# Kernel optimization log

Measured on AMD Instinct MI355X. Metric: run time of the kernel, lower is better.

Reference implementation:

```python
import jax, jax.numpy as jnp
import numpy as np

HEADS = 8
D_MODEL = 512

def setup_inputs() -> dict:
    key = jax.random.key(0)
    ks = jax.random.split(key, 7)
    t, w, h, b = 8, 14, 14, 8
    seq = t * w * h + 1  # 1569, includes CLS token
    q = jax.random.normal(ks[0], (seq, b, D_MODEL), jnp.float32)
    k = jax.random.normal(ks[1], (seq, b, D_MODEL), jnp.float32)
    value = jax.random.normal(ks[2], (seq, b, D_MODEL), jnp.float32)
    in_proj_weight = jax.random.normal(ks[3], (3 * D_MODEL, D_MODEL), jnp.float32) * (D_MODEL ** -0.5)
    in_proj_bias = jax.random.normal(ks[4], (3 * D_MODEL,), jnp.float32) * 0.02
    out_w = jax.random.normal(ks[5], (D_MODEL, D_MODEL), jnp.float32) * (D_MODEL ** -0.5)
    out_b = jax.random.normal(ks[6], (D_MODEL,), jnp.float32) * 0.02
    return {"q": q, "k": k, "value": value,
            "in_proj_weight": in_proj_weight, "in_proj_bias": in_proj_bias,
            "out_w": out_w, "out_b": out_b, "t": t, "w": w, "h": h}

def _sdpa(q, k, v):
    # scaled dot-product attention over batched 3D tensors [B, L, dh]
    temp = q.shape[-1] ** 0.5
    scores = jnp.einsum('bqd,bkd->bqk', q, k) / temp
    a = jax.nn.softmax(scores, axis=-1)  # softmax over dim=2 == last dim
    return jnp.einsum('bqk,bkd->bqd', a, v), a

def reference(q, k, value, in_proj_weight, in_proj_bias, out_w, out_b, t, w, h):
    seq, b, c = q.shape
    H, dh, wh = HEADS, c // HEADS, w * h
    q_cls = q[:1]          # [1, b, c] passed through untouched
    x = q[1:]              # [t*wh, b, c]
    qkv = x @ in_proj_weight.T + in_proj_bias  # fused QKV proj
    qq, kk, vv = qkv[..., :c], qkv[..., c:2 * c], qkv[..., 2 * c:]
    to5 = lambda z: z.reshape(t, wh, b, H, dh)
    # spatial stage: batch = (H, b, t), attend over wh
    q_s = to5(qq).transpose(3, 2, 0, 1, 4).reshape(H * b * t, wh, dh)
    k_s = to5(kk).transpose(3, 2, 0, 1, 4).reshape(H * b * t, wh, dh)
    v_s = to5(vv).transpose(3, 2, 0, 1, 4).reshape(H * b * t, wh, dh)
    out_s, attn = _sdpa(q_s, k_s, v_s)
    # temporal stage: batch = (H, b, wh), attend over t; V comes from spatial output
    v_t = out_s.reshape(H, b, t, wh, dh).transpose(0, 1, 3, 2, 4).reshape(H * b * wh, t, dh)
    q_t = to5(qq).transpose(3, 2, 1, 0, 4).reshape(H * b * wh, t, dh)
    k_t = to5(kk).transpose(3, 2, 1, 0, 4).reshape(H * b * wh, t, dh)
    out_t, _ = _sdpa(q_t, k_t, v_t)
    # back to [t*wh, b, c]
    out = out_t.reshape(H, b, wh, t, dh).transpose(3, 2, 1, 0, 4).reshape(t * wh, b, c)
    out = out @ out_w.T + out_b
    return jnp.concatenate([q_cls, out], axis=0), attn
```

## Files before the change

kernel.cpp:

```cpp
#include <hip/hip_runtime.h>
#include <cstdint>
#include <cstddef>

typedef __bf16 bf16;
typedef __bf16 bf16x8 __attribute__((ext_vector_type(8)));
typedef __bf16 bf16x4 __attribute__((ext_vector_type(4)));
typedef float  f32x4  __attribute__((ext_vector_type(4)));

#define MFMA16(a, b, c) __builtin_amdgcn_mfma_f32_16x16x32_bf16(a, b, c, 0, 0, 0)

__device__ __forceinline__ void gl2lds16(const bf16* g, bf16* l) {
  __builtin_amdgcn_global_load_lds(
      (const __attribute__((address_space(1))) void*)g,
      (__attribute__((address_space(3))) void*)l, 16, 0, 0);
}

__device__ __forceinline__ void cvt4(const float* __restrict__ s, bf16* __restrict__ d) {
  f32x4 v = *(const f32x4*)s;
  bf16x4 o;
  o[0] = (bf16)v[0]; o[1] = (bf16)v[1]; o[2] = (bf16)v[2]; o[3] = (bf16)v[3];
  *(bf16x4*)d = o;
}

__global__ __launch_bounds__(256) void prep_kernel(
    const float* __restrict__ q, const float* __restrict__ win,
    const float* __restrict__ wout, float* __restrict__ out0,
    bf16* __restrict__ xb, bf16* __restrict__ wqb, bf16* __restrict__ wob) {
  long u = (long)blockIdx.x * 256 + threadIdx.x;
  const long NX4 = 1605632, NWQ4 = 196608, NWO4 = 65536, NQC4 = 1024;
  if (u < NX4) { cvt4(q + 4096 + u * 4, xb + u * 4); return; }
  u -= NX4;
  if (u < NWQ4) { cvt4(win + u * 4, wqb + u * 4); return; }
  u -= NWQ4;
  if (u < NWO4) { cvt4(wout + u * 4, wob + u * 4); return; }
  u -= NWO4;
  if (u < NQC4) { *(f32x4*)(out0 + u * 4) = *(const f32x4*)(q + u * 4); }
}

template <bool OUTF32>
__global__ __launch_bounds__(256) void gemm_bt(
    const bf16* __restrict__ A, const bf16* __restrict__ Bm,
    const float* __restrict__ bias, bf16* __restrict__ Qh,
    bf16* __restrict__ Kh, bf16* __restrict__ Vh,
    float* __restrict__ Cf, int N, int K, long coff) {
  __shared__ bf16 As[128 * 64];
  __shared__ bf16 Bs[128 * 64];
  const int tid = threadIdx.x;
  const int wid = tid >> 6, lane = tid & 63;
  const int lr = lane & 15, lg = lane >> 4;

  const int nwg = gridDim.x * gridDim.y;
  const int orig = blockIdx.y * gridDim.x + blockIdx.x;
  const int cpx = nwg >> 3;
  const int swz = (orig & 7) * cpx + (orig >> 3);
  const int m0 = (swz / gridDim.x) * 128;
  const int n0 = (swz % gridDim.x) * 128;

  const int wr = wid >> 1, wc = wid & 1;
  const int slot = lane & 7, r8 = lane >> 3;
  const int chunk = slot ^ r8;
  const int x7 = lr & 7;

  f32x4 acc[4][4] = {};

  for (int kt = 0; kt < K; kt += 64) {
    __syncthreads();
#pragma unroll
    for (int j = 0; j < 4; ++j) {
      int blk = wid * 4 + j;
      int row = blk * 8 + r8;
      gl2lds16(A + (size_t)(m0 + row) * K + kt + chunk * 8, As + blk * 512);
      gl2lds16(Bm + (size_t)(n0 + row) * K + kt + chunk * 8, Bs + blk * 512);
    }
    __syncthreads();

#pragma unroll
    for (int kk = 0; kk < 2; ++kk) {
      bf16x8 af[4], bfr[4];
#pragma unroll
      for (int m = 0; m < 4; ++m)
        af[m] = *(const bf16x8*)(As + (wr * 64 + m * 16 + lr) * 64 +
                                 (((kk * 4 + lg) ^ x7) * 8));
#pragma unroll
      for (int n = 0; n < 4; ++n)
        bfr[n] = *(const bf16x8*)(Bs + (wc * 64 + n * 16 + lr) * 64 +
                                  (((kk * 4 + lg) ^ x7) * 8));
#pragma unroll
      for (int m = 0; m < 4; ++m)
#pragma unroll
        for (int n = 0; n < 4; ++n)
          acc[m][n] = MFMA16(af[m], bfr[n], acc[m][n]);
    }
  }

  if (OUTF32) {
#pragma unroll
    for (int m = 0; m < 4; ++m) {
      int row = m0 + wr * 64 + m * 16 + lg * 4;
#pragma unroll
      for (int n = 0; n < 4; ++n) {
        int col = n0 + wc * 64 + n * 16 + lr;
        float bv = bias[col];
#pragma unroll
        for (int i = 0; i < 4; ++i)
          __builtin_nontemporal_store(
              acc[m][n][i] + bv, Cf + coff + (size_t)(row + i) * N + col);
      }
    }
  } else {
    int off[4][4];
#pragma unroll
    for (int m = 0; m < 4; ++m)
#pragma unroll
      for (int i = 0; i < 4; ++i) {
        int r = m0 + wr * 64 + m * 16 + lg * 4 + i;
        int ti2 = r / 1568, rem = r - ti2 * 1568;
        off[m][i] = (int)(((rem & 7) * 8 + ti2) * 12544 + (rem >> 3) * 64);
      }
#pragma unroll
    for (int n = 0; n < 4; ++n) {
      int col = n0 + wc * 64 + n * 16 + lr;
      float bv = bias[col];
      int sec = col >> 9, c = col & 511;
      int hh = c >> 6, dd = c & 63;
      bf16* base = (sec == 0 ? Qh : (sec == 1 ? Kh : Vh)) +
                   (size_t)hh * 802816 + dd;
#pragma unroll
      for (int m = 0; m < 4; ++m)
#pragma unroll
        for (int i = 0; i < 4; ++i)
          base[off[m][i]] = (bf16)(acc[m][n][i] + bv);
    }
  }
}

__global__ __launch_bounds__(1024) void spatial_attn(
    const bf16* __restrict__ Qh, const bf16* __restrict__ Kh,
    const bf16* __restrict__ Vh, float* __restrict__ attn_out,
    bf16* __restrict__ outs) {
  __shared__ bf16 Kl[224 * 64];
  __shared__ bf16 Vt[64][232];
  __shared__ bf16 StgB[13 * 3136];

  const int tid = threadIdx.x;
  const int wid = tid >> 6, lane = tid & 63;
  const int lr = lane & 15, lg = lane >> 4;
  const int batch = blockIdx.x;
  const bf16* slabQ = Qh + (size_t)batch * 12544;
  const bf16* slabK = Kh + (size_t)batch * 12544;
  const bf16* slabV = Vh + (size_t)batch * 12544;

  {
    const int slot = lane & 7, r8 = lane >> 3;
    const int chunk = slot ^ r8;
#pragma unroll
    for (int t = 0; t < 2; ++t) {
      int j = wid + t * 16;
      if (j < 28) {
        int row = j * 8 + r8;
        int grow = row > 195 ? 195 : row;
        gl2lds16(slabK + grow * 64 + chunk * 8, Kl + j * 512);
      }
    }
  }
  {
    const int c = (wid & 7) * 8;
    const int rbase = (wid >> 3) * 64 + lane;
#pragma unroll
    for (int r0 = 0; r0 < 256; r0 += 128) {
      int pp = r0 + rbase;
      if (pp < 224) {
        int gp = pp > 195 ? 195 : pp;
        bf16x8 vv = *(const bf16x8*)(slabV + gp * 64 + c);
#pragma unroll
        for (int j = 0; j < 8; ++j) Vt[c + j][pp] = vv[j];
      }
    }
  }

  const int qt = wid;
  bf16x8 aq[2];
  if (qt < 13) {
    int row = qt * 16 + lr;
    if (row > 195) row = 195;
#pragma unroll
    for (int kk = 0; kk < 2; ++kk)
      aq[kk] = *(const bf16x8*)(slabQ + row * 64 + kk * 32 + lg * 8);
  }
  __syncthreads();

  if (qt < 13) {
    const int q = qt * 16 + lr;
    const int x7 = lr & 7;

    f32x4 s[14] = {};
    __builtin_amdgcn_s_setprio(1);
#pragma unroll
    for (int nn = 0; nn < 14; ++nn) {
      const int krow = nn * 16 + lr;
      bf16x8 bk0 = *(const bf16x8*)&Kl[krow * 64 + ((lg ^ x7) * 8)];
      bf16x8 bk1 = *(const bf16x8*)&Kl[krow * 64 + (((4 + lg) ^ x7) * 8)];
      s[nn] = MFMA16(bk0, aq[0], s[nn]);
      s[nn] = MFMA16(bk1, aq[1], s[nn]);
    }
    __builtin_amdgcn_s_setprio(0);

#pragma unroll
    for (int nn = 0; nn < 14; ++nn) {
      bool pad = (nn * 16 + lg * 4 >= 196);
#pragma unroll
      for (int i = 0; i < 4; ++i)
        s[nn][i] = pad ? -1e30f : s[nn][i] * 0.125f;
    }

    float v = -1e30f;
#pragma unroll
    for (int nn = 0; nn < 14; ++nn)
#pragma unroll
      for (int i = 0; i < 4; ++i) v = fmaxf(v, s[nn][i]);
    v = fmaxf(v, __shfl_xor(v, 16));
    v = fmaxf(v, __shfl_xor(v, 32));
    float sum = 0.f;
#pragma unroll
    for (int nn = 0; nn < 14; ++nn)
#pragma unroll
      for (int i = 0; i < 4; ++i) {
        float e = __expf(s[nn][i] - v);
        s[nn][i] = e;
        sum += e;
      }
    sum += __shfl_xor(sum, 16);
    sum += __shfl_xor(sum, 32);
    const float rinv = 1.f / sum;

    bf16* const tile = StgB + qt * 3136;
    const int low = lr + 32 * (lg & 1);
    const int high = low + 16;
    const bool hiN = (lg >> 1) != 0;
    f32x4 o[4] = {};
#pragma unroll
    for (int kb = 0; kb < 7; ++kb) {
      uint32_t px[2], py[2];
#pragma unroll
      for (int t = 0; t < 2; ++t) {
        const int nn = 2 * kb + t;
        f32x4 sv;
#pragma unroll
        for (int i = 0; i < 4; ++i) sv[i] = s[nn][i] * rinv;
        union { bf16x4 h; uint2 u; } pk;
        pk.h[0] = (bf16)sv[0]; pk.h[1] = (bf16)sv[1];
        pk.h[2] = (bf16)sv[2]; pk.h[3] = (bf16)sv[3];
        int kbase = nn * 16 + lg * 4;
        if (kbase < 196)
          *(uint2*)((char*)tile + lr * 392 + kbase * 2) = pk.u;
        px[t] = pk.u.x; py[t] = pk.u.y;
      }
      uint32_t a0x = __shfl((int)px[0], low);
      uint32_t a0y = __shfl((int)py[0], low);
      uint32_t a1x = __shfl((int)px[1], low);
      uint32_t a1y = __shfl((int)py[1], low);
      uint32_t b0x = __shfl((int)px[0], high);
      uint32_t b0y = __shfl((int)py[0], high);
      uint32_t b1x = __shfl((int)px[1], high);
      uint32_t b1y = __shfl((int)py[1], high);
      union { uint32_t u[4]; bf16x8 h; } pa;
      pa.u[0] = hiN ? a1x : a0x;
      pa.u[1] = hiN ? a1y : a0y;
      pa.u[2] = hiN ? b1x : b0x;
      pa.u[3] = hiN ? b1y : b0y;
      __builtin_amdgcn_s_setprio(1);
#pragma unroll
      for (int nd = 0; nd < 4; ++nd) {
        bf16x8 vb = *(const bf16x8*)&Vt[nd * 16 + lr][kb * 32 + lg * 8];
        o[nd] = MFMA16(pa.h, vb, o[nd]);
      }
      __builtin_amdgcn_s_setprio(0);
    }

    {
      const int hb8 = batch >> 3;
      const int ti = batch & 7;
#pragma unroll
      for (int i = 0; i < 4; ++i) {
        int p = qt * 16 + lg * 4 + i;
        if (p < 196) {
#pragma unroll
          for (int nd = 0; nd < 4; ++nd) {
            int d = nd * 16 + lr;
            outs[(((size_t)(hb8 * 196 + p)) * 8 + ti) * 64 + d] =
                (bf16)o[nd][i];
          }
        }
      }
    }

    {
      const int vbytes = (qt == 12) ? 3136 : 12544;
      char* dst = (char*)(attn_out + (size_t)batch * 38416 + qt * 3136);
      const char* src = (const char*)tile;
#pragma unroll
      for (int j = 0; j < 13; ++j) {
        int x = j * 1024 + lane * 16;
        if (x < vbytes) {
          uint2 u = *(const uint2*)(src + (x >> 1));
          union { uint32_t b; float f; } c0, c1, c2, c3;
          c0.b = (u.x & 0xffffu) << 16; c1.b = u.x & 0xffff0000u;
          c2.b = (u.y & 0xffffu) << 16; c3.b = u.y & 0xffff0000u;
          f32x4 ov; ov[0] = c0.f; ov[1] = c1.f; ov[2] = c2.f; ov[3] = c3.f;
          *(f32x4*)(dst + x) = ov;
        }
      }
    }
  }
}

__global__ __launch_bounds__(256) void temporal_attn(
    const bf16* __restrict__ Qh, const bf16* __restrict__ Kh,
    const bf16* __restrict__ outs, bf16* __restrict__ outt) {
  __shared__ bf16 Ql[4][8][72];
  __shared__ bf16 Kc[4][8][72];
  __shared__ bf16 Vl[4][8][64];
  __shared__ float Ps[4][8][8];

  const int tid = threadIdx.x, wid = tid >> 6, lane = tid & 63;
  const int batch = blockIdx.x * 4 + wid;
  const int p = batch % 196;
  const int hb = batch / 196;
  const int bb = hb & 7, h = hb >> 3;

  const int ri = lane >> 3;
  const int c8 = lane & 7;
  {
    size_t so = ((size_t)(h * 64 + bb * 8 + ri)) * 12544 + p * 64 + c8 * 8;
    *(bf16x8*)&Ql[wid][ri][c8 * 8] = *(const bf16x8*)(Qh + so);
    *(bf16x8*)&Kc[wid][ri][c8 * 8] = *(const bf16x8*)(Kh + so);
    *(bf16x8*)&Vl[wid][ri][c8 * 8] =
        *(const bf16x8*)(outs + ((size_t)batch * 8 + ri) * 64 + c8 * 8);
  }
  __syncthreads();

  float s = 0.f;
#pragma unroll
  for (int d = 0; d < 64; d += 8) {
    bf16x8 qv = *(const bf16x8*)&Ql[wid][ri][d];
    bf16x8 kv = *(const bf16x8*)&Kc[wid][c8][d];
#pragma unroll
    for (int e = 0; e < 8; ++e) s += (float)qv[e] * (float)kv[e];
  }
  s *= 0.125f;
  float mxv = s;
#pragma unroll
  for (int d2 = 1; d2 < 8; d2 <<= 1) mxv = fmaxf(mxv, __shfl_xor(mxv, d2));
  float e = __expf(s - mxv);
  float sum = e;
#pragma unroll
  for (int d2 = 1; d2 < 8; d2 <<= 1) sum += __shfl_xor(sum, d2);
  Ps[wid][ri][c8] = e / sum;
  __syncthreads();

  const int d = lane;
#pragma unroll
  for (int ii = 0; ii < 8; ++ii) {
    float o = 0.f;
#pragma unroll
    for (int j = 0; j < 8; ++j) o += Ps[wid][ii][j] * (float)Vl[wid][j][d];
    outt[((size_t)(ii * 196 + p) * 8 + bb) * 512 + h * 64 + d] = (bf16)o;
  }
}

extern "C" void kernel_launch(void* const* d_in, const int* in_sizes, int n_in,
                              void* d_out, int out_size, void* d_ws,
                              size_t ws_size, hipStream_t stream) {
  (void)in_sizes; (void)n_in; (void)out_size; (void)ws_size;
  const float* q    = (const float*)d_in[0];
  const float* win  = (const float*)d_in[3];
  const float* bin  = (const float*)d_in[4];
  const float* wout = (const float*)d_in[5];
  const float* bout = (const float*)d_in[6];
  float* out0 = (float*)d_out;
  float* attn = out0 + 6426624L;

  bf16* Qh   = (bf16*)d_ws;
  bf16* Kh   = Qh + 6422528L;
  bf16* Vh   = Kh + 6422528L;
  bf16* outs = Vh + 6422528L;
  bf16* outt = outs + 6422528L;
  bf16* wob  = outt + 6422528L;

  bf16* xb  = (bf16*)attn;
  bf16* wqb = xb + 6422528L;

  prep_kernel<<<7300, 256, 0, stream>>>(q, win, wout, out0, xb, wqb, wob);
  gemm_bt<false><<<dim3(12, 98), 256, 0, stream>>>(
      xb, wqb, bin, Qh, Kh, Vh, nullptr, 1536, 512, 0);
  spatial_attn<<<512, 1024, 0, stream>>>(Qh, Kh, Vh, attn, outs);
  temporal_attn<<<3136, 256, 0, stream>>>(Qh, Kh, outs, outt);
  gemm_bt<true><<<dim3(4, 98), 256, 0, stream>>>(
      outt, wob, bout, nullptr, nullptr, nullptr, out0, 512, 512, 4096);
}
```

Before: 95.89 us.

## Fuse QKV projection GEMM into spatial attention kernel

Removes the separate QKV projection GEMM launch. Each spatial attention block now computes its own head's Q, K and V tile from the bf16 input and weight slices, staged through LDS, and feeds them straight into attention. Only Q and K are written back to global memory for the temporal stage, and the V round-trip is eliminated. In exchange, each 1024-thread block runs a K-loop GEMM with 13 of its 16 waves active. The weight slices are also re-read by every block, and the staging buffers are relocated into the output region.

```diff
diff --git a/kernel.cpp b/kernel.cpp
--- a/kernel.cpp
+++ b/kernel.cpp
@@ -37,12 +37,10 @@
   if (u < NQC4) { *(f32x4*)(out0 + u * 4) = *(const f32x4*)(q + u * 4); }
 }
 
-template <bool OUTF32>
 __global__ __launch_bounds__(256) void gemm_bt(
     const bf16* __restrict__ A, const bf16* __restrict__ Bm,
-    const float* __restrict__ bias, bf16* __restrict__ Qh,
-    bf16* __restrict__ Kh, bf16* __restrict__ Vh,
-    float* __restrict__ Cf, int N, int K, long coff) {
+    const float* __restrict__ bias, float* __restrict__ Cf,
+    int N, int K, long coff) {
   __shared__ bf16 As[128 * 64];
   __shared__ bf16 Bs[128 * 64];
   const int tid = threadIdx.x;
@@ -93,113 +91,145 @@
     }
   }
 
-  if (OUTF32) {
-#pragma unroll
-    for (int m = 0; m < 4; ++m) {
-      int row = m0 + wr * 64 + m * 16 + lg * 4;
-#pragma unroll
-      for (int n = 0; n < 4; ++n) {
-        int col = n0 + wc * 64 + n * 16 + lr;
-        float bv = bias[col];
-#pragma unroll
-        for (int i = 0; i < 4; ++i)
-          __builtin_nontemporal_store(
-              acc[m][n][i] + bv, Cf + coff + (size_t)(row + i) * N + col);
-      }
-    }
-  } else {
-    int off[4][4];
-#pragma unroll
-    for (int m = 0; m < 4; ++m)
-#pragma unroll
-      for (int i = 0; i < 4; ++i) {
-        int r = m0 + wr * 64 + m * 16 + lg * 4 + i;
-        int ti2 = r / 1568, rem = r - ti2 * 1568;
-        off[m][i] = (int)(((rem & 7) * 8 + ti2) * 12544 + (rem >> 3) * 64);
-      }
+#pragma unroll
+  for (int m = 0; m < 4; ++m) {
+    int row = m0 + wr * 64 + m * 16 + lg * 4;
 #pragma unroll
     for (int n = 0; n < 4; ++n) {
       int col = n0 + wc * 64 + n * 16 + lr;
       float bv = bias[col];
-      int sec = col >> 9, c = col & 511;
-      int hh = c >> 6, dd = c & 63;
-      bf16* base = (sec == 0 ? Qh : (sec == 1 ? Kh : Vh)) +
-                   (size_t)hh * 802816 + dd;
-#pragma unroll
-      for (int m = 0; m < 4; ++m)
-#pragma unroll
-        for (int i = 0; i < 4; ++i)
-          base[off[m][i]] = (bf16)(acc[m][n][i] + bv);
-    }
-  }
-}
-
-__global__ __launch_bounds__(1024) void spatial_attn(
-    const bf16* __restrict__ Qh, const bf16* __restrict__ Kh,
-    const bf16* __restrict__ Vh, float* __restrict__ attn_out,
+#pragma unroll
+      for (int i = 0; i < 4; ++i)
+        __builtin_nontemporal_store(
+            acc[m][n][i] + bv, Cf + coff + (size_t)(row + i) * N + col);
+    }
+  }
+}
+
+__global__ __launch_bounds__(1024) void spatial_fused(
+    const bf16* __restrict__ xb, const bf16* __restrict__ wqb,
+    const float* __restrict__ bin, bf16* __restrict__ Qh,
+    bf16* __restrict__ Kh, float* __restrict__ attn_out,
     bf16* __restrict__ outs) {
-  __shared__ bf16 Kl[224 * 64];
-  __shared__ bf16 Vt[64][232];
-  __shared__ bf16 StgB[13 * 3136];
+  __shared__ bf16 Kl[224 * 72];
+  __shared__ bf16 Vt[64 * 232];
+  __shared__ bf16 RB[40768];
+  bf16* const Xs  = RB;
+  bf16* const Wss = RB + 13312;
+  bf16* const Qb  = RB + 25600;
+  bf16* const StgB = RB;
 
   const int tid = threadIdx.x;
   const int wid = tid >> 6, lane = tid & 63;
   const int lr = lane & 15, lg = lane >> 4;
   const int batch = blockIdx.x;
-  const bf16* slabQ = Qh + (size_t)batch * 12544;
-  const bf16* slabK = Kh + (size_t)batch * 12544;
-  const bf16* slabV = Vh + (size_t)batch * 12544;
-
-  {
-    const int slot = lane & 7, r8 = lane >> 3;
-    const int chunk = slot ^ r8;
-#pragma unroll
-    for (int t = 0; t < 2; ++t) {
-      int j = wid + t * 16;
-      if (j < 28) {
-        int row = j * 8 + r8;
-        int grow = row > 195 ? 195 : row;
-        gl2lds16(slabK + grow * 64 + chunk * 8, Kl + j * 512);
-      }
-    }
-  }
-  {
-    const int c = (wid & 7) * 8;
-    const int rbase = (wid >> 3) * 64 + lane;
-#pragma unroll
-    for (int r0 = 0; r0 < 256; r0 += 128) {
-      int pp = r0 + rbase;
-      if (pp < 224) {
-        int gp = pp > 195 ? 195 : pp;
-        bf16x8 vv = *(const bf16x8*)(slabV + gp * 64 + c);
-#pragma unroll
-        for (int j = 0; j < 8; ++j) Vt[c + j][pp] = vv[j];
-      }
-    }
-  }
-
+  const int h = batch >> 6;
+  const int bb = (batch >> 3) & 7;
+  const int ti = batch & 7;
+
+  { int d = tid >> 4, r = 208 + (tid & 15); Vt[d * 232 + r] = (bf16)0.f; }
+
+  const int r8 = lane >> 3, slot = lane & 7;
+  const int chunk = slot ^ r8;
   const int qt = wid;
+  const int x7 = lr & 7;
+
+  f32x4 acc[12] = {};
+
+  for (int kt = 0; kt < 512; kt += 64) {
+    __syncthreads();
+#pragma unroll
+    for (int t = 0; t < 4; ++t) {
+      int task = wid + t * 16;
+      if (task < 26) {
+        int row = task * 8 + r8;
+        int xr = row > 195 ? 195 : row;
+        gl2lds16(xb + ((size_t)(ti * 196 + xr) * 8 + bb) * 512 + kt +
+                     chunk * 8,
+                 Xs + task * 512);
+      } else if (task < 50) {
+        int j = task - 26;
+        int strip = j >> 3;
+        int wrow = strip * 512 + h * 64 + (j & 7) * 8 + r8;
+        gl2lds16(wqb + (size_t)wrow * 512 + kt + chunk * 8, Wss + j * 512);
+      }
+    }
+    __syncthreads();
+    if (qt < 13) {
+#pragma unroll
+      for (int kk = 0; kk < 2; ++kk) {
+        bf16x8 af = *(const bf16x8*)(Xs + (qt * 16 + lr) * 64 +
+                                     (((kk * 4 + lg) ^ x7) * 8));
+#pragma unroll
+        for (int nf = 0; nf < 12; ++nf) {
+          bf16x8 bfr = *(const bf16x8*)(Wss + (nf * 16 + lr) * 64 +
+                                        (((kk * 4 + lg) ^ x7) * 8));
+          acc[nf] = MFMA16(af, bfr, acc[nf]);
+        }
+      }
+    }
+  }
+
   bf16x8 aq[2];
   if (qt < 13) {
-    int row = qt * 16 + lr;
-    if (row > 195) row = 195;
+#pragma unroll
+    for (int nf = 0; nf < 12; ++nf) {
+      int strip = nf >> 2;
+      float bv = bin[strip * 512 + h * 64 + (nf & 3) * 16 + lr];
+#pragma unroll
+      for (int i = 0; i < 4; ++i) acc[nf][i] += bv;
+    }
+    bf16* qb = Qb + qt * 1152;
+#pragma unroll
+    for (int nf = 0; nf < 4; ++nf)
+#pragma unroll
+      for (int i = 0; i < 4; ++i)
+        qb[(lg * 4 + i) * 72 + nf * 16 + lr] = (bf16)acc[nf][i];
+#pragma unroll
+    for (int nf = 4; nf < 8; ++nf)
+#pragma unroll
+      for (int i = 0; i < 4; ++i)
+        Kl[(qt * 16 + lg * 4 + i) * 72 + (nf - 4) * 16 + lr] =
+            (bf16)acc[nf][i];
+#pragma unroll
+    for (int nf = 8; nf < 12; ++nf) {
+      union { bf16x4 h4; uint2 u; } pk;
+      pk.h4[0] = (bf16)acc[nf][0]; pk.h4[1] = (bf16)acc[nf][1];
+      pk.h4[2] = (bf16)acc[nf][2]; pk.h4[3] = (bf16)acc[nf][3];
+      int d = (nf - 8) * 16 + lr;
+      *(uint2*)&Vt[d * 232 + qt * 16 + lg * 4] = pk.u;
+    }
 #pragma unroll
     for (int kk = 0; kk < 2; ++kk)
-      aq[kk] = *(const bf16x8*)(slabQ + row * 64 + kk * 32 + lg * 8);
+      aq[kk] = *(const bf16x8*)(qb + lr * 72 + kk * 32 + lg * 8);
+    {
+      bf16* slabQ = Qh + (size_t)batch * 12544;
+      bf16* slabK = Kh + (size_t)batch * 12544;
+      const int erow = lane >> 3, eseg = lane & 7;
+#pragma unroll
+      for (int t = 0; t < 2; ++t) {
+        int row = qt * 16 + t * 8 + erow;
+        if (row < 196) {
+          bf16x8 qv = *(const bf16x8*)(qb + (t * 8 + erow) * 72 + eseg * 8);
+          *(bf16x8*)(slabQ + row * 64 + eseg * 8) = qv;
+          bf16x8 kv = *(const bf16x8*)(Kl + row * 72 + eseg * 8);
+          *(bf16x8*)(slabK + row * 64 + eseg * 8) = kv;
+        }
+      }
+    }
   }
   __syncthreads();
 
   if (qt < 13) {
     const int q = qt * 16 + lr;
-    const int x7 = lr & 7;
 
     f32x4 s[14] = {};
     __builtin_amdgcn_s_setprio(1);
 #pragma unroll
     for (int nn = 0; nn < 14; ++nn) {
       const int krow = nn * 16 + lr;
-      bf16x8 bk0 = *(const bf16x8*)&Kl[krow * 64 + ((lg ^ x7) * 8)];
-      bf16x8 bk1 = *(const bf16x8*)&Kl[krow * 64 + (((4 + lg) ^ x7) * 8)];
+      bf16x8 bk0 = *(const bf16x8*)&Kl[krow * 72 + lg * 8];
+      bf16x8 bk1 = *(const bf16x8*)&Kl[krow * 72 + 32 + lg * 8];
       s[nn] = MFMA16(bk0, aq[0], s[nn]);
       s[nn] = MFMA16(bk1, aq[1], s[nn]);
     }
@@ -247,9 +277,9 @@
         f32x4 sv;
 #pragma unroll
         for (int i = 0; i < 4; ++i) sv[i] = s[nn][i] * rinv;
-        union { bf16x4 h; uint2 u; } pk;
-        pk.h[0] = (bf16)sv[0]; pk.h[1] = (bf16)sv[1];
-        pk.h[2] = (bf16)sv[2]; pk.h[3] = (bf16)sv[3];
+        union { bf16x4 h4; uint2 u; } pk;
+        pk.h4[0] = (bf16)sv[0]; pk.h4[1] = (bf16)sv[1];
+        pk.h4[2] = (bf16)sv[2]; pk.h4[3] = (bf16)sv[3];
         int kbase = nn * 16 + lg * 4;
         if (kbase < 196)
           *(uint2*)((char*)tile + lr * 392 + kbase * 2) = pk.u;
@@ -263,7 +293,7 @@
       uint32_t b0y = __shfl((int)py[0], high);
       uint32_t b1x = __shfl((int)px[1], high);
       uint32_t b1y = __shfl((int)py[1], high);
-      union { uint32_t u[4]; bf16x8 h; } pa;
+      union { uint32_t u[4]; bf16x8 h8; } pa;
       pa.u[0] = hiN ? a1x : a0x;
       pa.u[1] = hiN ? a1y : a0y;
       pa.u[2] = hiN ? b1x : b0x;
@@ -271,15 +301,14 @@
       __builtin_amdgcn_s_setprio(1);
 #pragma unroll
       for (int nd = 0; nd < 4; ++nd) {
-        bf16x8 vb = *(const bf16x8*)&Vt[nd * 16 + lr][kb * 32 + lg * 8];
-        o[nd] = MFMA16(pa.h, vb, o[nd]);
+        bf16x8 vb = *(const bf16x8*)&Vt[(nd * 16 + lr) * 232 + kb * 32 + lg * 8];
+        o[nd] = MFMA16(pa.h8, vb, o[nd]);
       }
       __builtin_amdgcn_s_setprio(0);
     }
 
     {
       const int hb8 = batch >> 3;
-      const int ti = batch & 7;
 #pragma unroll
       for (int i = 0; i < 4; ++i) {
         int p = qt * 16 + lg * 4 + i;
@@ -382,19 +411,16 @@
 
   bf16* Qh   = (bf16*)d_ws;
   bf16* Kh   = Qh + 6422528L;
-  bf16* Vh   = Kh + 6422528L;
-  bf16* outs = Vh + 6422528L;
+  bf16* outs = Kh + 6422528L;
   bf16* outt = outs + 6422528L;
   bf16* wob  = outt + 6422528L;
-
-  bf16* xb  = (bf16*)attn;
-  bf16* wqb = xb + 6422528L;
+  bf16* xb   = wob + 262144L;
+
+  bf16* wqb = (bf16*)(out0 + 4096);
 
   prep_kernel<<<7300, 256, 0, stream>>>(q, win, wout, out0, xb, wqb, wob);
-  gemm_bt<false><<<dim3(12, 98), 256, 0, stream>>>(
-      xb, wqb, bin, Qh, Kh, Vh, nullptr, 1536, 512, 0);
-  spatial_attn<<<512, 1024, 0, stream>>>(Qh, Kh, Vh, attn, outs);
+  spatial_fused<<<512, 1024, 0, stream>>>(xb, wqb, bin, Qh, Kh, attn, outs);
   temporal_attn<<<3136, 256, 0, stream>>>(Qh, Kh, outs, outt);
-  gemm_bt<true><<<dim3(4, 98), 256, 0, stream>>>(
-      outt, wob, bout, nullptr, nullptr, nullptr, out0, 512, 512, 4096);
-}
+  gemm_bt<<<dim3(4, 98), 256, 0, stream>>>(outt, wob, bout, out0, 512, 512,
+                                           4096);
+}
```

After: 92.27 us. 1.04x faster.
